# Performance work log

Measured on AMD Instinct MI355X. Metric: run time of the kernel, lower is better.

The kernel has to match this reference:

```python
import jax, jax.numpy as jnp
import numpy as np

B, WS, DIM, HEADS, AGENT, PS = 128, 14, 256, 8, 49, 7
N = WS * WS


def conv(x, w, b, pad, groups=1):
    y = jax.lax.conv_general_dilated(x, w, (1, 1), [(pad, pad), (pad, pad)],
                                     dimension_numbers=('NCHW', 'OIHW', 'NCHW'),
                                     feature_group_count=groups)
    return y + b[None, :, None, None]


def bilinear_resize(x, oh, ow):
    # F.interpolate(mode='bilinear', align_corners=False) on last two dims
    ih, iw = x.shape[-2], x.shape[-1]
    def grid(ni, no):
        pos = np.maximum((np.arange(no) + 0.5) * (ni / no) - 0.5, 0.0)
        i0 = np.minimum(np.floor(pos).astype(np.int32), ni - 1)
        i1 = np.minimum(i0 + 1, ni - 1)
        return i0, i1, (pos - i0).astype(np.float32)
    i0h, i1h, lh = grid(ih, oh)
    i0w, i1w, lw = grid(iw, ow)
    xh = x[..., i0h, :] * (1.0 - lh)[:, None] + x[..., i1h, :] * lh[:, None]
    return xh[..., i0w] * (1.0 - lw) + xh[..., i1w] * lw


def rel_pos_index(h, w):
    coords = np.stack(np.meshgrid(np.arange(h), np.arange(w), indexing='ij')).reshape(2, -1)
    rel = (coords[:, :, None] - coords[:, None, :]).transpose(1, 2, 0).copy()
    rel[..., 0] += h - 1
    rel[..., 1] += w - 1
    rel[..., 0] *= 2 * w - 1
    return rel.sum(-1)  # (h*w, h*w)


def cbam(x, caa1_w, caa1_b, caa2_w, caa2_b, cam1_w, cam1_b, cam2_w, cam2_b, sa_w, sa_b):
    # ChannelAttention: both conv stacks act on 1x1 pooled maps -> only kernel centers matter
    avgp = x.mean((2, 3))
    t1 = jax.nn.relu(jnp.einsum('oi,bi->bo', caa1_w[:, :, 1, 1], avgp) + caa1_b)
    y1 = jax.nn.sigmoid(jnp.einsum('oi,bi->bo', caa2_w[:, :, 1, 1], t1) + caa2_b)
    mxp = x.max((2, 3))
    t2 = jax.nn.relu(jnp.einsum('oi,bi->bo', cam1_w[:, :, 0, 0], mxp) + cam1_b)
    y2 = jax.nn.sigmoid(jnp.einsum('oi,bi->bo', cam2_w[:, :, 0, 0], t2) + cam2_b)
    x = jax.nn.sigmoid(y1 + y2)[:, :, None, None] * x
    # Spatial attention
    mask = jnp.concatenate([x.mean(1, keepdims=True), x.max(1, keepdims=True)], axis=1)
    mask = jax.nn.sigmoid(conv(mask, sa_w, sa_b, 4))
    return x * mask


def chan_inter(x, ci1_w, ci1_b, bn_g, bn_b, ci2_w, ci2_b):
    # AdaptiveAvgPool2d(1) then 5x5 convs on 1x1 maps -> kernel-center matmuls; BN in eval mode
    p = x.mean((2, 3))
    t = jnp.einsum('oi,bi->bo', ci1_w[:, :, 2, 2], p) + ci1_b
    t = jax.nn.relu(bn_g * t * (1.0 / np.sqrt(1.0 + 1e-5)) + bn_b)
    return jnp.einsum('oi,bi->bo', ci2_w[:, :, 2, 2], t) + ci2_b


def setup_inputs() -> dict:
    key = jax.random.key(0)
    ks = jax.random.split(key, 40)
    d, r = DIM, DIM // 16
    p = lambda i, shape, s=0.02: jax.random.normal(ks[i], shape, jnp.float32) * s
    return {
        'x': jax.random.normal(ks[0], (B, N, d), jnp.float32),
        'h': WS,
        'w': WS,
        'lka_w': p(1, (3 * d, 1, 5, 5)), 'lka_b': p(2, (3 * d,)),
        'conv5_w': p(3, (d, d, 5, 5)), 'conv5_b': p(4, (d,)),
        'caa1_w': p(5, (r, d, 3, 3)), 'caa1_b': p(6, (r,)),
        'caa2_w': p(7, (d, r, 3, 3)), 'caa2_b': p(8, (d,)),
        'cam1_w': p(9, (r, d, 1, 1)), 'cam1_b': p(10, (r,)),
        'cam2_w': p(11, (d, r, 1, 1)), 'cam2_b': p(12, (d,)),
        'sa_w': p(13, (1, 2, 9, 9)), 'sa_b': p(14, (1,)),
        'ci1_w': p(15, (r, d, 5, 5)), 'ci1_b': p(16, (r,)),
        'bn_g': jnp.ones((r,), jnp.float32), 'bn_b': jnp.zeros((r,), jnp.float32),
        'ci2_w': p(17, (d, r, 5, 5)), 'ci2_b': p(18, (d,)),
        'rpb_table': p(19, ((2 * WS - 1) * (2 * WS - 1), HEADS)),
        'an_bias': p(20, (HEADS, AGENT, 7, 7)), 'na_bias': p(21, (HEADS, AGENT, 7, 7)),
        'ah_bias': p(22, (1, HEADS, AGENT, WS, 1)), 'aw_bias': p(23, (1, HEADS, AGENT, 1, WS)),
        'ha_bias': p(24, (1, HEADS, WS, 1, AGENT)), 'wa_bias': p(25, (1, HEADS, 1, WS, AGENT)),
        'dwc_w': p(26, (d, 1, 5, 5)), 'dwc_b': p(27, (d,)),
        'proj_w': p(28, (d, d)), 'proj_b': p(29, (d,)),
    }


def reference(x, h, w, lka_w, lka_b, conv5_w, conv5_b, caa1_w, caa1_b, caa2_w, caa2_b,
              cam1_w, cam1_b, cam2_w, cam2_b, sa_w, sa_b, ci1_w, ci1_b, bn_g, bn_b,
              ci2_w, ci2_b, rpb_table, an_bias, na_bias, ah_bias, aw_bias, ha_bias,
              wa_bias, dwc_w, dwc_b, proj_w, proj_b):
    b, n, c = x.shape
    heads, agent, ps = HEADS, AGENT, PS
    hd = c // heads
    scale = hd ** (-0.5)

    xc = jnp.transpose(x.reshape(b, h, w, c), (0, 3, 1, 2))  # (b,c,h,w)
    y = conv(xc, lka_w, lka_b, 2, groups=c)                   # depthwise, 3 outputs/group
    k_raw, v_raw, q_raw = y[:, :c], y[:, c:2 * c], y[:, 2 * c:]

    # v branch: conv5 then raw reshape-scramble (faithful to torch .reshape of NCHW), then CBAM
    v5 = jnp.transpose(conv(v_raw, conv5_w, conv5_b, 2).reshape(b, h, w, c), (0, 3, 1, 2))
    vc = cbam(v5, caa1_w, caa1_b, caa2_w, caa2_b, cam1_w, cam1_b, cam2_w, cam2_b, sa_w, sa_b)
    v_feat = jnp.transpose(vc.reshape(b, c, n), (0, 2, 1))    # (b,n,c)

    # adaptive avg/max pool 14->7 == exact 2x2 pooling
    at = q_raw.reshape(b, c, ps, h // ps, ps, w // ps).mean((3, 5)).reshape(b, c, agent).transpose(0, 2, 1)
    atk = k_raw.reshape(b, c, ps, h // ps, ps, w // ps).max((3, 5)).reshape(b, c, agent).transpose(0, 2, 1)

    # raw row-major reshapes of (b,c,h,w) into (b,n,heads,hd): faithful to torch
    q = q_raw.reshape(b, n, heads, hd).transpose(0, 2, 1, 3) * scale
    k = k_raw.reshape(b, n, heads, hd).transpose(0, 2, 1, 3)
    v = v_raw.reshape(b, n, heads, hd).transpose(0, 2, 1, 3)
    v1 = v_feat.reshape(b, n, heads, hd).transpose(0, 2, 1, 3)

    # full window attention with relative position bias
    idx = rel_pos_index(h, w)
    rpb = rpb_table[idx.reshape(-1)].reshape(n, n, heads).transpose(2, 0, 1)
    attn = jax.nn.softmax(jnp.einsum('bhid,bhjd->bhij', q, k) + rpb[None])
    x1 = jnp.einsum('bhij,bhjd->bhid', attn, v).transpose(0, 2, 1, 3).reshape(b, n, c)

    ar = x1.transpose(0, 2, 1).reshape(b, c, h, w)
    cmap = chan_inter(ar, ci1_w, ci1_b, bn_g, bn_b, ci2_w, ci2_b)  # (b,c)
    conv_x2 = jax.nn.sigmoid(cmap)[:, :, None, None] * jnp.transpose(q.reshape(b, h, w, c), (0, 3, 1, 2))

    # agent attention
    at_h = at.reshape(b, agent, heads, hd).transpose(0, 2, 1, 3)
    atk_h = atk.reshape(b, agent, heads, hd).transpose(0, 2, 1, 3)
    pb = bilinear_resize(an_bias, h, w).reshape(1, heads, agent, n) \
         + (ah_bias + aw_bias).reshape(1, heads, agent, n)
    agent_attn = jax.nn.softmax(jnp.einsum('bhad,bhnd->bhan', at_h * scale, k) + pb)
    agent_attn1 = jax.nn.softmax(jnp.einsum('bhad,bhnd->bhan', atk_h * scale, q) + pb)
    agent_v = jnp.einsum('bhan,bhnd->bhad', agent_attn, v1) + jnp.einsum('bhan,bhnd->bhad', agent_attn1, v)

    ab = bilinear_resize(na_bias, h, w).reshape(1, heads, agent, n).transpose(0, 1, 3, 2) \
         + (ha_bias + wa_bias).reshape(1, heads, n, agent)
    q_attn = jax.nn.softmax(jnp.einsum('bhnd,bhad->bhna', q * scale, at_h) + ab)
    k_attn = jax.nn.softmax(jnp.einsum('bhnd,bhad->bhna', k * scale, atk_h) + ab)
    xo = jnp.einsum('bhna,bhad->bhnd', q_attn + k_attn, agent_v).transpose(0, 2, 1, 3).reshape(b, n, c)

    xo = xo + jnp.transpose(conv(conv_x2, dwc_w, dwc_b, 2, groups=c), (0, 2, 3, 1)).reshape(b, n, c)
    qc = jnp.transpose(q.transpose(0, 2, 1, 3).reshape(b, h, w, c), (0, 3, 1, 2))
    xo = xo + jnp.transpose(conv(qc, dwc_w, dwc_b, 2, groups=c), (0, 2, 3, 1)).reshape(b, n, c)

    return xo @ proj_w.T + proj_b
```

## Files before the change

kernel.cpp:

```cpp
#include <hip/hip_runtime.h>

#define NB    128
#define NC    256
#define NPOS  196
#define NHEAD 8
#define NAG   49
#define YSTR  150528
#define VOFF  50176
#define QOFF  100352
#define SCL   0.17677669529663687f

#define WS_Y    0u
#define WS_V5   19267584u
#define WS_AT   25690112u
#define WS_ATK  27295744u
#define WS_CHG  28901376u
#define WS_CMAP 28934144u
#define WS_PBT  28966912u
#define WS_AB   29043744u
#define WS_X1S  29120576u
#define WS_AGV  29153344u
#define WS_XO   30758976u
#define WS_WT   37181504u
#define WS_CWT  37247040u

typedef __attribute__((ext_vector_type(8))) _Float16 half8;
typedef __attribute__((ext_vector_type(8))) short short8;
typedef __attribute__((ext_vector_type(4))) short short4v;
typedef __attribute__((ext_vector_type(4))) float f32x4;
typedef unsigned short ushort_t;
typedef unsigned int uint_t;

__device__ __forceinline__ float sigmoidf_(float x){ return 1.0f/(1.0f+__expf(-x)); }

__device__ __forceinline__ ushort_t f2h(float x){
  _Float16 h = (_Float16)x; return __builtin_bit_cast(ushort_t, h);
}
__device__ __forceinline__ float h2f(ushort_t u){
  return (float)__builtin_bit_cast(_Float16, u);
}

__device__ __forceinline__ float bilin7(const float* __restrict__ src, int i, int j){
  float pi = fmaxf(0.5f*(float)i - 0.25f, 0.f);
  int i0 = (int)pi; if (i0 > 6) i0 = 6;
  int i1 = i0 + 1;  if (i1 > 6) i1 = 6;
  float li = pi - (float)i0;
  float pj = fmaxf(0.5f*(float)j - 0.25f, 0.f);
  int j0 = (int)pj; if (j0 > 6) j0 = 6;
  int j1 = j0 + 1;  if (j1 > 6) j1 = 6;
  float lj = pj - (float)j0;
  float v00 = src[i0*7+j0], v01 = src[i0*7+j1];
  float v10 = src[i1*7+j0], v11 = src[i1*7+j1];
  float t0 = v00*(1.f-lj) + v01*lj;
  float t1 = v10*(1.f-lj) + v11*lj;
  return t0*(1.f-li) + t1*li;
}

__device__ __forceinline__ void conv5x5_row(const float* __restrict__ plane, int r,
                                            const float* __restrict__ w25, float* acc14){
  #pragma unroll
  for (int di = 0; di < 5; ++di){
    const float4* pr = (const float4*)(plane + (r+di)*20);
    float4 p0 = pr[0], p1 = pr[1], p2 = pr[2], p3 = pr[3], p4 = pr[4];
    float row[20] = {p0.x,p0.y,p0.z,p0.w, p1.x,p1.y,p1.z,p1.w, p2.x,p2.y,p2.z,p2.w,
                     p3.x,p3.y,p3.z,p3.w, p4.x,p4.y,p4.z,p4.w};
    #pragma unroll
    for (int dj = 0; dj < 5; ++dj){
      float w = w25[di*5+dj];
      #pragma unroll
      for (int j = 0; j < 14; ++j) acc14[j] = fmaf(row[j+dj], w, acc14[j]);
    }
  }
}

__global__ void k_pb(const float* __restrict__ an, const float* __restrict__ ah,
                     const float* __restrict__ aw, float* __restrict__ PBT){
  int t = blockIdx.x*256 + threadIdx.x;
  if (t >= NHEAD*NPOS*NAG) return;
  int a = t % NAG;
  int r = t / NAG;
  int n = r % NPOS;
  int h = r / NPOS;
  int i = n/14, j = n - (n/14)*14;
  float v = bilin7(an + ((size_t)h*NAG + a)*49, i, j);
  v += ah[((size_t)h*NAG + a)*14 + i] + aw[((size_t)h*NAG + a)*14 + j];
  PBT[t] = v;
}

__global__ void k_ab(const float* __restrict__ na, const float* __restrict__ ha,
                     const float* __restrict__ wa, float* __restrict__ AB){
  int t = blockIdx.x*256 + threadIdx.x;
  if (t >= NHEAD*NPOS*NAG) return;
  int a = t % NAG;
  int r = t / NAG;
  int n = r % NPOS;
  int h = r / NPOS;
  int i = n/14, j = n - (n/14)*14;
  float v = bilin7(na + ((size_t)h*NAG + a)*49, i, j);
  v += ha[((size_t)h*14 + i)*NAG + a] + wa[((size_t)h*14 + j)*NAG + a];
  AB[t] = v;
}

__global__ void k_wt(const float* __restrict__ pw, float* __restrict__ WT){
  int t = blockIdx.x*256 + threadIdx.x;
  if (t >= 65536) return;
  int k = t >> 8, c = t & 255;
  WT[t] = pw[c*256 + k];
}

__global__ void k_cw2(const float* __restrict__ cw, ushort_t* __restrict__ Wh){
  int t = blockIdx.x*256 + threadIdx.x;
  if (t >= 1638400) return;
  int ci = t & 255;
  int r  = t >> 8;
  int co = r & 255;
  int tap = r >> 8;
  Wh[t] = f2h(cw[((size_t)co*256 + ci)*25 + tap]);
}

__global__ __launch_bounds__(256) void k_lka(const float* __restrict__ x, const float* __restrict__ lw,
                                             const float* __restrict__ lb, float* __restrict__ Y){
  int b = blockIdx.x >> 3, gb = blockIdx.x & 7;
  int g0 = gb*32;
  __shared__ __align__(16) float pl[32*360];
  int tid = threadIdx.x;
  for (int t = tid; t < 32*360; t += 256) pl[t] = 0.f;
  __syncthreads();
  for (int t = tid; t < 32*196; t += 256){
    int gl = t & 31, s = t >> 5;
    int i = s/14, j = s - i*14;
    pl[gl*360 + (i+2)*20 + j + 2] = x[((size_t)b*196 + s)*256 + g0 + gl];
  }
  __syncthreads();
  for (int t = tid; t < 96*14; t += 256){
    int ocl = t/14, r = t - ocl*14;
    int o  = g0*3 + ocl;
    int gl = ocl/3;
    float w25[25];
    #pragma unroll
    for (int u = 0; u < 25; ++u) w25[u] = lw[o*25 + u];
    float acc[14];
    float bv = lb[o];
    #pragma unroll
    for (int j = 0; j < 14; ++j) acc[j] = bv;
    conv5x5_row(&pl[gl*360], r, w25, acc);
    float* dst = Y + ((size_t)b*768 + o)*196 + r*14;
    #pragma unroll
    for (int j = 0; j < 14; ++j) dst[j] = acc[j];
  }
}

__global__ __launch_bounds__(256, 2) void k_conv5(const float* __restrict__ Y,
    const ushort_t* __restrict__ Wh, const float* __restrict__ cb, float* __restrict__ V5){
  int b = blockIdx.x >> 2, cog = blockIdx.x & 3;
  int co0 = cog*64;
  __shared__ __align__(16) ushort_t Pt[360*40];
  __shared__ __align__(16) ushort_t Wsm[5*64*40];
  __shared__ float T[32*200];
  int tid  = threadIdx.x;
  int lane = tid & 63, wv = tid >> 6;
  int mrow = lane & 15, quad = lane >> 4;

  for (int t = tid; t < 7200; t += 256) ((uint_t*)Pt)[t] = 0;

  int prow[4];
  #pragma unroll
  for (int mt = 0; mt < 4; ++mt){
    int s = wv*64 + mt*16 + mrow;
    int p0 = 0;
    if (s < 196){ int i = s/14, j = s - i*14; p0 = i*20 + j; }
    prow[mt] = p0;
  }

  f32x4 acc[4][4];
  #pragma unroll
  for (int mt = 0; mt < 4; ++mt)
    #pragma unroll
    for (int nt = 0; nt < 4; ++nt) acc[mt][nt] = (f32x4){0.f,0.f,0.f,0.f};

  const float* src = Y + (size_t)b*YSTR + VOFF;
  int wco = tid >> 2, wpart = tid & 3;

  #pragma unroll 1
  for (int cc = 0; cc < 8; ++cc){
    __syncthreads();
    for (int t = tid; t < 3136; t += 256){
      int cp = t / 196, s = t - cp*196;
      int i = s/14, j = s - i*14;
      const float* s0 = src + (size_t)(cc*32 + 2*cp)*196 + s;
      float v0 = s0[0];
      float v1 = s0[196];
      ((uint_t*)Pt)[((i+2)*20 + j + 2)*20 + cp] =
          (uint_t)f2h(v0) | ((uint_t)f2h(v1) << 16);
    }
    #pragma unroll 1
    for (int di = 0; di < 5; ++di){
      __syncthreads();
      #pragma unroll
      for (int tp = 0; tp < 5; ++tp){
        int tap = di*5 + tp;
        const short8 g = *(const short8*)(Wh + ((size_t)tap*256 + co0 + wco)*256 + cc*32 + wpart*8);
        *(short8*)&Wsm[(tp*64 + wco)*40 + wpart*8] = g;
      }
      __syncthreads();
      #pragma unroll
      for (int dj = 0; dj < 5; ++dj){
        half8 a[4], bb[4];
        #pragma unroll
        for (int nt = 0; nt < 4; ++nt){
          int co = nt*16 + mrow;
          bb[nt] = *(const half8*)&Wsm[(dj*64 + co)*40 + quad*8];
        }
        #pragma unroll
        for (int mt = 0; mt < 4; ++mt){
          int p = prow[mt] + di*20 + dj;
          a[mt] = *(const half8*)&Pt[p*40 + quad*8];
        }
        #pragma unroll
        for (int mt = 0; mt < 4; ++mt)
          #pragma unroll
          for (int nt = 0; nt < 4; ++nt)
            acc[mt][nt] = __builtin_amdgcn_mfma_f32_16x16x32_f16(a[mt], bb[nt], acc[mt][nt], 0, 0, 0);
      }
    }
  }

  #pragma unroll
  for (int hf = 0; hf < 2; ++hf){
    __syncthreads();
    #pragma unroll
    for (int ntl = 0; ntl < 2; ++ntl){
      int nt = hf*2 + ntl;
      int col = ntl*16 + mrow;
      #pragma unroll
      for (int mt = 0; mt < 4; ++mt){
        int sbase = wv*64 + mt*16 + quad*4;
        #pragma unroll
        for (int r = 0; r < 4; ++r){
          int s = sbase + r;
          if (s < 196) T[col*200 + s] = acc[mt][nt][r];
        }
      }
    }
    __syncthreads();
    for (int t = tid; t < 6272; t += 256){
      int cl = t / 196;
      int f = (co0 + hf*32)*196 + t;
      float val = T[t + cl*4] + cb[co0 + hf*32 + cl];
      V5[(size_t)b*50176 + (size_t)(f & 255)*196 + (f >> 8)] = val;
    }
  }
}

__global__ __launch_bounds__(256) void k_pool(const float* __restrict__ Y, float* __restrict__ AT, float* __restrict__ ATK){
  int b = blockIdx.x; int c = threadIdx.x;
  const float* qp = Y + ((size_t)b*768 + 512 + c)*196;
  const float* kp = Y + ((size_t)b*768 + c)*196;
  for (int a = 0; a < 49; ++a){
    int p1 = a/7, p2 = a - p1*7;
    int s = p1*28 + p2*2;
    float q0 = qp[s], q1 = qp[s+1], q2 = qp[s+14], q3 = qp[s+15];
    AT[((size_t)b*49 + a)*256 + c] = 0.25f*(q0+q1+q2+q3);
    float k0 = kp[s], k1 = kp[s+1], k2 = kp[s+14], k3 = kp[s+15];
    ATK[((size_t)b*49 + a)*256 + c] = fmaxf(fmaxf(k0,k1), fmaxf(k2,k3));
  }
}

__global__ __launch_bounds__(256) void k_cbam_a(const float* __restrict__ V5,
    const float* __restrict__ caa1w, const float* __restrict__ caa1b,
    const float* __restrict__ caa2w, const float* __restrict__ caa2b,
    const float* __restrict__ cam1w, const float* __restrict__ cam1b,
    const float* __restrict__ cam2w, const float* __restrict__ cam2b,
    float* __restrict__ CHG){
  int b = blockIdx.x, c = threadIdx.x;
  __shared__ float avg[256], mx[256], t1[16], t2[16];
  const float* pp = V5 + ((size_t)b*256 + c)*196;
  float s = 0.f, m = -1e30f;
  for (int i = 0; i < 196; ++i){ float v = pp[i]; s += v; m = fmaxf(m, v); }
  avg[c] = s * (1.0f/196.0f); mx[c] = m;
  __syncthreads();
  if (c < 16){
    float a1 = caa1b[c], a2 = cam1b[c];
    #pragma unroll 4
    for (int k = 0; k < 256; ++k){
      a1 = fmaf(caa1w[(c*256 + k)*9 + 4], avg[k], a1);
      a2 = fmaf(cam1w[c*256 + k], mx[k], a2);
    }
    t1[c] = fmaxf(a1, 0.f);
    t2[c] = fmaxf(a2, 0.f);
  }
  __syncthreads();
  float y1 = caa2b[c], y2 = cam2b[c];
  #pragma unroll
  for (int k = 0; k < 16; ++k){
    y1 = fmaf(caa2w[(c*16 + k)*9 + 4], t1[k], y1);
    y2 = fmaf(cam2w[c*16 + k], t2[k], y2);
  }
  CHG[b*256 + c] = sigmoidf_(sigmoidf_(y1) + sigmoidf_(y2));
}

__global__ __launch_bounds__(256) void k_cbam_b(float* __restrict__ V5, const float* __restrict__ CHG,
    const float* __restrict__ saw, const float* __restrict__ sab){
  int b = blockIdx.x; int tid = threadIdx.x;
  __shared__ float chg[256];
  __shared__ float mp[22*22], xp[22*22];
  __shared__ float mk[196];
  chg[tid] = CHG[b*256 + tid];
  for (int t = tid; t < 484; t += 256){ mp[t] = 0.f; xp[t] = 0.f; }
  __syncthreads();
  if (tid < 196){
    int i = tid/14, j = tid - i*14;
    float s = 0.f, m = -1e30f;
    const float* vb = V5 + (size_t)b*256*196 + tid;
    for (int c = 0; c < 256; ++c){
      float v = chg[c] * vb[c*196];
      s += v; m = fmaxf(m, v);
    }
    mp[(i+4)*22 + j+4] = s*(1.f/256.f);
    xp[(i+4)*22 + j+4] = m;
  }
  __syncthreads();
  if (tid < 196){
    int i = tid/14, j = tid - i*14;
    float acc = sab[0];
    for (int di = 0; di < 9; ++di){
      #pragma unroll
      for (int dj = 0; dj < 9; ++dj){
        acc = fmaf(mp[(i+di)*22 + j+dj], saw[di*9+dj], acc);
        acc = fmaf(xp[(i+di)*22 + j+dj], saw[81 + di*9+dj], acc);
      }
    }
    mk[tid] = sigmoidf_(acc);
  }
  __syncthreads();
  if (tid < 196){
    float m = mk[tid];
    float* vb = V5 + (size_t)b*256*196 + tid;
    for (int c = 0; c < 256; ++c) vb[c*196] = chg[c]*vb[c*196]*m;
  }
}

__global__ __launch_bounds__(256) void k_attn(const float* __restrict__ Y, const float* __restrict__ rpbt,
                                              float* __restrict__ X1S){
  int b = blockIdx.x >> 3, h = blockIdx.x & 7;
  __shared__ float rp[729];
  __shared__ float xs[196*33];
  int tid = threadIdx.x;
  for (int t = tid; t < 729; t += 256) rp[t] = rpbt[t*8 + h];
  __syncthreads();
  const float* yb = Y + (size_t)b*YSTR;
  if (tid < 196){
    int n = tid;
    float q[32];
    {
      const float4* q4 = (const float4*)(yb + QOFF + (size_t)n*256 + h*32);
      #pragma unroll
      for (int u = 0; u < 8; ++u){
        float4 v = q4[u];
        q[4*u] = v.x*SCL; q[4*u+1] = v.y*SCL; q[4*u+2] = v.z*SCL; q[4*u+3] = v.w*SCL;
      }
    }
    int ri = n/14, ci = n - ri*14;
    int bidx = (ri + 13)*27 + (ci + 13);
    float acc[32];
    #pragma unroll
    for (int d = 0; d < 32; ++d) acc[d] = 0.f;
    float l = 0.f;
    int rj = 0, cj = 0;
    for (int j = 0; j < 196; ++j){
      const float4* k4 = (const float4*)(yb + (size_t)j*256 + h*32);
      float s0 = 0.f, s1 = 0.f;
      #pragma unroll
      for (int u = 0; u < 8; u += 2){
        float4 a = k4[u], bb = k4[u+1];
        s0 = fmaf(q[4*u+0],a.x, fmaf(q[4*u+1],a.y, fmaf(q[4*u+2],a.z, fmaf(q[4*u+3],a.w, s0))));
        s1 = fmaf(q[4*u+4],bb.x, fmaf(q[4*u+5],bb.y, fmaf(q[4*u+6],bb.z, fmaf(q[4*u+7],bb.w, s1))));
      }
      float s = s0 + s1 + rp[bidx - rj*27 - cj];
      float p = __expf(s);
      l += p;
      const float4* v4 = (const float4*)(yb + VOFF + (size_t)j*256 + h*32);
      #pragma unroll
      for (int u = 0; u < 8; ++u){
        float4 vv = v4[u];
        acc[4*u]   = fmaf(p, vv.x, acc[4*u]);
        acc[4*u+1] = fmaf(p, vv.y, acc[4*u+1]);
        acc[4*u+2] = fmaf(p, vv.z, acc[4*u+2]);
        acc[4*u+3] = fmaf(p, vv.w, acc[4*u+3]);
      }
      if (++cj == 14){ cj = 0; ++rj; }
    }
    float inv = 1.f/l;
    #pragma unroll
    for (int d = 0; d < 32; ++d) xs[n*33 + d] = acc[d]*inv;
  }
  __syncthreads();
  if (tid < 32){
    float s = 0.f;
    for (int n = 0; n < 196; ++n) s += xs[n*33 + tid];
    X1S[(size_t)b*256 + h*32 + tid] = s*(1.f/196.f);
  }
}

__global__ __launch_bounds__(256) void k_cinter(const float* __restrict__ X1S,
    const float* __restrict__ ci1w, const float* __restrict__ ci1b,
    const float* __restrict__ bng, const float* __restrict__ bnb,
    const float* __restrict__ ci2w, const float* __restrict__ ci2b, float* __restrict__ CMAP){
  int b = blockIdx.x, c = threadIdx.x;
  __shared__ float p[256], tt[16];
  p[c] = X1S[b*256 + c];
  __syncthreads();
  if (c < 16){
    float a = ci1b[c];
    #pragma unroll 4
    for (int k = 0; k < 256; ++k) a = fmaf(ci1w[(c*256+k)*25 + 12], p[k], a);
    const float invs = 0.9999950000375f;
    tt[c] = fmaxf(fmaf(bng[c]*invs, a, bnb[c]), 0.f);
  }
  __syncthreads();
  float a = ci2b[c];
  #pragma unroll
  for (int k = 0; k < 16; ++k) a = fmaf(ci2w[(c*16+k)*25 + 12], tt[k], a);
  CMAP[b*256 + c] = sigmoidf_(a);
}

__global__ __launch_bounds__(256) void k_agentv(const float* __restrict__ Y, const float* __restrict__ V5,
    const float* __restrict__ AT, const float* __restrict__ ATK,
    const float* __restrict__ PBT, float* __restrict__ AGV){
  int b = blockIdx.x >> 3, h = blockIdx.x & 7;
  __shared__ __align__(16) ushort_t ST[64*232];
  __shared__ __align__(16) ushort_t R[8704];
  __shared__ float psum[4*64];
  __shared__ float inv0s[64], inv1s[64];
  int tid = threadIdx.x, wv = tid >> 6, lane = tid & 63;
  int mrow = lane & 15, quad = lane >> 4;
  int sw8 = ((quad ^ ((mrow >> 1) & 3)) << 3);
  const float* yb = Y + (size_t)b*YSTR;
  ushort_t* Kh = R;
  ushort_t* Ah = R + 6656;
  ushort_t* Vt = R;
  f32x4 out0[2], out1[2];

  for (int t = tid; t < 512; t += 256){
    int a = t >> 3, c2 = 208 + ((t & 7) << 1);
    *(uint_t*)&ST[a*232 + c2] = 0;
  }

  #pragma unroll 1
  for (int pass = 0; pass < 2; ++pass){
    for (int t = tid; t < 192; t += 256) ((uint_t*)Kh)[3136 + t] = 0;
    for (int t = tid; t < 240; t += 256) ((uint_t*)Ah)[784 + t] = 0;
    {
      const float* rsrc = yb + (pass ? QOFF : 0) + h*32;
      for (int t = tid; t < 3136; t += 256){
        int n = t >> 4, w = t & 15;
        const float2 v = *(const float2*)(rsrc + (size_t)n*256 + (w << 1));
        int ws = (((w >> 2) ^ ((n >> 1) & 3)) << 2) | (w & 3);
        ((uint_t*)Kh)[n*16 + ws] = (uint_t)f2h(v.x) | ((uint_t)f2h(v.y) << 16);
      }
      const float* asrc = (pass ? ATK : AT) + (size_t)b*49*256 + h*32;
      for (int t = tid; t < 784; t += 256){
        int a = t >> 4, w = t & 15;
        const float2 v = *(const float2*)(asrc + (size_t)a*256 + (w << 1));
        int ws = (((w >> 2) ^ ((a >> 1) & 3)) << 2) | (w & 3);
        ((uint_t*)Ah)[a*16 + ws] = (uint_t)f2h(v.x) | ((uint_t)f2h(v.y) << 16);
      }
    }
    __syncthreads();
    {
      float lscl = pass ? 0.03125f : SCL;
      int ag = wv*16 + mrow;
      half8 bfr = *(const half8*)&Ah[ag*32 + sw8];
      #pragma unroll 1
      for (int mt = 0; mt < 13; ++mt){
        half8 afr = *(const half8*)&Kh[(mt*16 + mrow)*32 + sw8];
        f32x4 c = (f32x4){0.f,0.f,0.f,0.f};
        c = __builtin_amdgcn_mfma_f32_16x16x32_f16(afr, bfr, c, 0, 0, 0);
        int n0 = mt*16 + quad*4;
        short4v pk;
        #pragma unroll
        for (int r = 0; r < 4; ++r){
          int n = n0 + r;
          float pb = PBT[((size_t)h*196 + n)*49 + ag];
          float e = (n < 196) ? __expf(fmaf(c[r], lscl, pb)) : 0.f;
          pk[r] = (short)f2h(e);
        }
        *(short4v*)&ST[ag*232 + n0] = pk;
      }
    }
    __syncthreads();
    {
      int a = tid >> 2, q = tid & 3;
      float s = 0.f;
      #pragma unroll
      for (int u = 0; u < 7; ++u){
        short8 v8 = *(const short8*)&ST[a*232 + q*56 + u*8];
        #pragma unroll
        for (int e = 0; e < 8; ++e) s += h2f((ushort_t)v8[e]);
      }
      psum[q*64 + a] = s;
    }
    if (pass == 0){
      const float* vsrc = V5 + (size_t)b*50176 + h*32*196;
      for (int t = tid; t < 3136; t += 256){
        int d = t / 98, np = t - (t/98)*98;
        const float2 v = *(const float2*)(vsrc + (size_t)d*196 + 2*np);
        *(uint_t*)&Vt[d*232 + 2*np] = (uint_t)f2h(v.x) | ((uint_t)f2h(v.y) << 16);
      }
    } else {
      const float* vsrc = yb + VOFF + h*32;
      for (int t = tid; t < 3136; t += 256){
        int d = t / 98, np = t - (t/98)*98;
        float v0 = vsrc[(size_t)(2*np)*256 + d];
        float v1 = vsrc[(size_t)(2*np+1)*256 + d];
        *(uint_t*)&Vt[d*232 + 2*np] = (uint_t)f2h(v0) | ((uint_t)f2h(v1) << 16);
      }
    }
    for (int t = tid; t < 448; t += 256){
      int d = t / 14, c2 = 196 + 2*(t - (t/14)*14);
      *(uint_t*)&Vt[d*232 + c2] = 0;
    }
    __syncthreads();
    {
      f32x4* outp = pass ? out1 : out0;
      #pragma unroll
      for (int nt = 0; nt < 2; ++nt){
        f32x4 c = (f32x4){0.f,0.f,0.f,0.f};
        #pragma unroll
        for (int ks = 0; ks < 7; ++ks){
          half8 afr = *(const half8*)&ST[(wv*16 + mrow)*232 + ks*32 + quad*8];
          half8 bfr = *(const half8*)&Vt[(nt*16 + mrow)*232 + ks*32 + quad*8];
          c = __builtin_amdgcn_mfma_f32_16x16x32_f16(afr, bfr, c, 0, 0, 0);
        }
        outp[nt] = c;
      }
      if (tid < 64){
        float s = psum[tid] + psum[64+tid] + psum[128+tid] + psum[192+tid];
        float* invp = pass ? inv1s : inv0s;
        invp[tid] = 1.f / s;
      }
    }
    __syncthreads();
  }
  #pragma unroll
  for (int nt = 0; nt < 2; ++nt){
    int d = nt*16 + mrow;
    #pragma unroll
    for (int r = 0; r < 4; ++r){
      int a = wv*16 + quad*4 + r;
      if (a < 49)
        AGV[(((size_t)(b*8 + h)*49) + a)*32 + d] = out0[nt][r]*inv0s[a] + out1[nt][r]*inv1s[a];
    }
  }
}

__global__ __launch_bounds__(256) void k_xo1(const float* __restrict__ Y,
    const float* __restrict__ AT, const float* __restrict__ ATK,
    const float* __restrict__ AB, const float* __restrict__ AGV, float* __restrict__ XO){
  int b = blockIdx.x >> 3, h = blockIdx.x & 7;
  __shared__ __align__(16) ushort_t ST[208*72];
  __shared__ __align__(16) ushort_t Kh[208*32];
  __shared__ __align__(16) ushort_t Ah[64*32];
  __shared__ __align__(16) ushort_t AGVt[32*64];
  __shared__ float invs[208];
  int tid = threadIdx.x, wv = tid >> 6, lane = tid & 63;
  int mrow = lane & 15, quad = lane >> 4;
  int sw8 = ((quad ^ ((mrow >> 1) & 3)) << 3);
  const float* yb = Y + (size_t)b*YSTR;
  f32x4 acc[4][2];
  #pragma unroll
  for (int i = 0; i < 4; ++i){
    acc[i][0] = (f32x4){0.f,0.f,0.f,0.f};
    acc[i][1] = (f32x4){0.f,0.f,0.f,0.f};
  }

  for (int t = tid; t < 1664; t += 256){
    int rw = t >> 3, c2 = 48 + ((t & 7) << 1);
    *(uint_t*)&ST[rw*72 + c2] = 0;
  }
  {
    const float* agvb = AGV + (size_t)(b*8 + h)*49*32;
    for (int t = tid; t < 2048; t += 256){
      int d = t >> 6, a = t & 63;
      int as = ((((a >> 3) ^ (d & 7)) & 7) << 3) | (a & 7);
      AGVt[d*64 + as] = (a < 49) ? f2h(agvb[a*32 + d]) : (ushort_t)0;
    }
  }

  #pragma unroll 1
  for (int pass = 0; pass < 2; ++pass){
    {
      const float* rsrc = yb + (pass ? 0 : QOFF) + h*32;
      for (int t = tid; t < 3136; t += 256){
        int n = t >> 4, w = t & 15;
        const float2 v = *(const float2*)(rsrc + (size_t)n*256 + (w << 1));
        int ws = (((w >> 2) ^ ((n >> 1) & 3)) << 2) | (w & 3);
        ((uint_t*)Kh)[n*16 + ws] = (uint_t)f2h(v.x) | ((uint_t)f2h(v.y) << 16);
      }
      const float* asrc = (pass ? ATK : AT) + (size_t)b*49*256 + h*32;
      for (int t = tid; t < 784; t += 256){
        int a = t >> 4, w = t & 15;
        const float2 v = *(const float2*)(asrc + (size_t)a*256 + (w << 1));
        int ws = (((w >> 2) ^ ((a >> 1) & 3)) << 2) | (w & 3);
        ((uint_t*)Ah)[a*16 + ws] = (uint_t)f2h(v.x) | ((uint_t)f2h(v.y) << 16);
      }
    }
    __syncthreads();
    {
      float lscl = pass ? SCL : 0.03125f;
      int ag = wv*16 + mrow;
      half8 bfr = *(const half8*)&Ah[ag*32 + sw8];
      #pragma unroll 1
      for (int mt = 0; mt < 13; ++mt){
        half8 afr = *(const half8*)&Kh[(mt*16 + mrow)*32 + sw8];
        f32x4 c = (f32x4){0.f,0.f,0.f,0.f};
        c = __builtin_amdgcn_mfma_f32_16x16x32_f16(afr, bfr, c, 0, 0, 0);
        #pragma unroll
        for (int r = 0; r < 4; ++r){
          int n = mt*16 + quad*4 + r;
          if (n < 196 && ag < 49){
            float e = __expf(fmaf(c[r], lscl, AB[((size_t)h*196 + n)*49 + ag]));
            ST[n*72 + ag] = f2h(e);
          }
        }
      }
    }
    __syncthreads();
    if (tid < 196){
      float s = 0.f;
      #pragma unroll
      for (int u = 0; u < 7; ++u){
        short8 v8 = *(const short8*)&ST[tid*72 + u*8];
        #pragma unroll
        for (int e = 0; e < 8; ++e) s += h2f((ushort_t)v8[e]);
      }
      invs[tid] = 1.f / s;
    }
    __syncthreads();
    {
      int i = 0;
      #pragma unroll 1
      for (int mt = wv; mt < 13; mt += 4, ++i){
        #pragma unroll
        for (int nt = 0; nt < 2; ++nt){
          f32x4 c = (f32x4){0.f,0.f,0.f,0.f};
          #pragma unroll
          for (int ks = 0; ks < 2; ++ks){
            half8 afr = *(const half8*)&ST[(mt*16 + mrow)*72 + ks*32 + quad*8];
            half8 bfr = *(const half8*)&AGVt[(nt*16 + mrow)*64 + ((((ks*4 + quad) ^ (mrow & 7)) & 7) << 3)];
            c = __builtin_amdgcn_mfma_f32_16x16x32_f16(afr, bfr, c, 0, 0, 0);
          }
          #pragma unroll
          for (int r = 0; r < 4; ++r){
            int n = mt*16 + quad*4 + r;
            if (n < 196) acc[i][nt][r] = fmaf(c[r], invs[n], acc[i][nt][r]);
          }
        }
      }
    }
    __syncthreads();
  }
  {
    int i = 0;
    #pragma unroll 1
    for (int mt = wv; mt < 13; mt += 4, ++i){
      #pragma unroll
      for (int nt = 0; nt < 2; ++nt){
        #pragma unroll
        for (int r = 0; r < 4; ++r){
          int n = mt*16 + quad*4 + r;
          if (n < 196)
            XO[((size_t)b*196 + n)*256 + h*32 + nt*16 + mrow] = acc[i][nt][r];
        }
      }
    }
  }
}

__global__ __launch_bounds__(256) void k_dwc(const float* __restrict__ Y, const float* __restrict__ CMAP,
    const float* __restrict__ dw, const float* __restrict__ db, float* __restrict__ XO){
  int b = blockIdx.x >> 3, cg = blockIdx.x & 7;
  int c0 = cg*32;
  __shared__ __align__(16) float pl[32*360];
  int tid = threadIdx.x;
  for (int t = tid; t < 32*360; t += 256) pl[t] = 0.f;
  __syncthreads();
  const float* yq = Y + (size_t)b*YSTR + QOFF;
  for (int t = tid; t < 32*196; t += 256){
    int cl = t & 31, s = t >> 5;
    int c = c0 + cl;
    int G = s*256 + c;
    int hh = G / 6272;
    int rem = G - hh*6272;
    int n = rem >> 5, d = rem & 31;
    float cx2 = CMAP[b*256 + c] * yq[n*256 + hh*32 + d];
    float qc  = yq[G];
    float v = SCL*(cx2 + qc);
    int i = s/14, j = s - i*14;
    pl[cl*360 + (i+2)*20 + j + 2] = v;
  }
  __syncthreads();
  for (int t = tid; t < 32*14; t += 256){
    int cl = t/14, r = t - cl*14;
    int c = c0 + cl;
    float w25[25];
    #pragma unroll
    for (int u = 0; u < 25; ++u) w25[u] = dw[c*25 + u];
    float acc[14];
    float b2 = 2.f*db[c];
    #pragma unroll
    for (int j = 0; j < 14; ++j) acc[j] = b2;
    conv5x5_row(&pl[cl*360], r, w25, acc);
    float* dst = XO + ((size_t)b*196 + r*14)*256 + c;
    #pragma unroll
    for (int j = 0; j < 14; ++j) dst[j*256] += acc[j];
  }
}

__global__ __launch_bounds__(256) void k_proj(const float* __restrict__ XO, const float* __restrict__ WT,
    const float* __restrict__ pbias, float* __restrict__ OUT){
  int bb = blockIdx.x / 7, nt = blockIdx.x % 7;
  int n0 = nt*28;
  int c = threadIdx.x;
  const float* xb = XO + ((size_t)bb*196 + n0)*256;
  float acc[28];
  #pragma unroll
  for (int r = 0; r < 28; ++r) acc[r] = 0.f;
  for (int k = 0; k < 256; k += 4){
    float w0 = WT[(k+0)*256 + c];
    float w1 = WT[(k+1)*256 + c];
    float w2 = WT[(k+2)*256 + c];
    float w3 = WT[(k+3)*256 + c];
    #pragma unroll
    for (int r = 0; r < 28; ++r){
      float4 xv = *(const float4*)(xb + r*256 + k);
      acc[r] = fmaf(xv.x, w0, fmaf(xv.y, w1, fmaf(xv.z, w2, fmaf(xv.w, w3, acc[r]))));
    }
  }
  float bv = pbias[c];
  float* dst = OUT + ((size_t)bb*196 + n0)*256 + c;
  #pragma unroll
  for (int r = 0; r < 28; ++r) dst[r*256] = acc[r] + bv;
}

extern "C" void kernel_launch(void* const* d_in, const int* in_sizes, int n_in,
                              void* d_out, int out_size, void* d_ws, size_t ws_size,
                              hipStream_t stream){
  (void)in_sizes; (void)n_in; (void)out_size; (void)ws_size;
  const float* x       = (const float*)d_in[0];
  const float* lka_w   = (const float*)d_in[3];
  const float* lka_b   = (const float*)d_in[4];
  const float* conv5_w = (const float*)d_in[5];
  const float* conv5_b = (const float*)d_in[6];
  const float* caa1_w  = (const float*)d_in[7];
  const float* caa1_b  = (const float*)d_in[8];
  const float* caa2_w  = (const float*)d_in[9];
  const float* caa2_b  = (const float*)d_in[10];
  const float* cam1_w  = (const float*)d_in[11];
  const float* cam1_b  = (const float*)d_in[12];
  const float* cam2_w  = (const float*)d_in[13];
  const float* cam2_b  = (const float*)d_in[14];
  const float* sa_w    = (const float*)d_in[15];
  const float* sa_b    = (const float*)d_in[16];
  const float* ci1_w   = (const float*)d_in[17];
  const float* ci1_b   = (const float*)d_in[18];
  const float* bn_g    = (const float*)d_in[19];
  const float* bn_b    = (const float*)d_in[20];
  const float* ci2_w   = (const float*)d_in[21];
  const float* ci2_b   = (const float*)d_in[22];
  const float* rpbt    = (const float*)d_in[23];
  const float* an_bias = (const float*)d_in[24];
  const float* na_bias = (const float*)d_in[25];
  const float* ah_bias = (const float*)d_in[26];
  const float* aw_bias = (const float*)d_in[27];
  const float* ha_bias = (const float*)d_in[28];
  const float* wa_bias = (const float*)d_in[29];
  const float* dwc_w   = (const float*)d_in[30];
  const float* dwc_b   = (const float*)d_in[31];
  const float* proj_w  = (const float*)d_in[32];
  const float* proj_b  = (const float*)d_in[33];
  float* out = (float*)d_out;
  float* ws = (float*)d_ws;

  float* Y    = ws + WS_Y;
  float* V5   = ws + WS_V5;
  float* AT   = ws + WS_AT;
  float* ATK  = ws + WS_ATK;
  float* CHG  = ws + WS_CHG;
  float* CMAP = ws + WS_CMAP;
  float* PBT  = ws + WS_PBT;
  float* AB   = ws + WS_AB;
  float* X1S  = ws + WS_X1S;
  float* AGV  = ws + WS_AGV;
  float* XO   = ws + WS_XO;
  float* WT   = ws + WS_WT;
  ushort_t* Wh = (ushort_t*)(ws + WS_CWT);

  k_pb   <<<301, 256, 0, stream>>>(an_bias, ah_bias, aw_bias, PBT);
  k_ab   <<<301, 256, 0, stream>>>(na_bias, ha_bias, wa_bias, AB);
  k_wt   <<<256, 256, 0, stream>>>(proj_w, WT);
  k_cw2  <<<6400, 256, 0, stream>>>(conv5_w, Wh);
  k_lka  <<<1024, 256, 0, stream>>>(x, lka_w, lka_b, Y);
  k_conv5<<<512, 256, 0, stream>>>(Y, Wh, conv5_b, V5);
  k_pool <<<128, 256, 0, stream>>>(Y, AT, ATK);
  k_cbam_a<<<128, 256, 0, stream>>>(V5, caa1_w, caa1_b, caa2_w, caa2_b,
                                    cam1_w, cam1_b, cam2_w, cam2_b, CHG);
  k_cbam_b<<<128, 256, 0, stream>>>(V5, CHG, sa_w, sa_b);
  k_attn <<<1024, 256, 0, stream>>>(Y, rpbt, X1S);
  k_cinter<<<128, 256, 0, stream>>>(X1S, ci1_w, ci1_b, bn_g, bn_b, ci2_w, ci2_b, CMAP);
  k_agentv<<<1024, 256, 0, stream>>>(Y, V5, AT, ATK, PBT, AGV);
  k_xo1  <<<1024, 256, 0, stream>>>(Y, AT, ATK, AB, AGV, XO);
  k_dwc  <<<1024, 256, 0, stream>>>(Y, CMAP, dwc_w, dwc_b, XO);
  k_proj <<<896, 256, 0, stream>>>(XO, WT, proj_b, out);
}
```

Baseline: 895.4 us.

## Rewrite window attention with MFMA scores and mean-pooled reassociation; swizzle conv5 LDS

The window attention kernel now computes QK^T scores with fp16 MFMA, stores unnormalised exponentials in LDS, and uses the fact that only the mean over queries is needed. It sums the normalised attention weights per key first, then does a single weighted sum over V, which replaces the per-query PV accumulation. The conv5 kernel gets XOR-swizzled LDS layouts for the patch and weight tiles to avoid bank conflicts, a packed per-position staging loop, and skips the MFMAs for the padded rows in the last wave. This trades fp32 precision for fp16 in the scores and uses much more shared memory per block.

After: 870.0 us. -2.8%, faster.

```diff
diff --git a/kernel.cpp b/kernel.cpp
--- a/kernel.cpp
+++ b/kernel.cpp
@@ -160,6 +160,7 @@
   int tid  = threadIdx.x;
   int lane = tid & 63, wv = tid >> 6;
   int mrow = lane & 15, quad = lane >> 4;
+  int mtN  = (wv < 3) ? 4 : 1;
 
   for (int t = tid; t < 7200; t += 256) ((uint_t*)Pt)[t] = 0;
 
@@ -184,14 +185,18 @@
   #pragma unroll 1
   for (int cc = 0; cc < 8; ++cc){
     __syncthreads();
-    for (int t = tid; t < 3136; t += 256){
-      int cp = t / 196, s = t - cp*196;
-      int i = s/14, j = s - i*14;
-      const float* s0 = src + (size_t)(cc*32 + 2*cp)*196 + s;
-      float v0 = s0[0];
-      float v1 = s0[196];
-      ((uint_t*)Pt)[((i+2)*20 + j + 2)*20 + cp] =
-          (uint_t)f2h(v0) | ((uint_t)f2h(v1) << 16);
+    if (tid < 196){
+      int s = tid; int i = s/14, j = s - i*14;
+      int p = (i+2)*20 + (j+2);
+      const float* s0 = src + (cc*32)*196 + s;
+      #pragma unroll
+      for (int cp = 0; cp < 16; ++cp){
+        float v0 = s0[(2*cp)*196];
+        float v1 = s0[(2*cp+1)*196];
+        uint_t pk = (uint_t)f2h(v0) | ((uint_t)f2h(v1) << 16);
+        int q = cp >> 2;
+        *(uint_t*)&Pt[p*40 + (((q ^ p) & 3) << 3) + ((2*cp) & 7)] = pk;
+      }
     }
     #pragma unroll 1
     for (int di = 0; di < 5; ++di){
@@ -200,7 +205,7 @@
       for (int tp = 0; tp < 5; ++tp){
         int tap = di*5 + tp;
         const short8 g = *(const short8*)(Wh + ((size_t)tap*256 + co0 + wco)*256 + cc*32 + wpart*8);
-        *(short8*)&Wsm[(tp*64 + wco)*40 + wpart*8] = g;
+        *(short8*)&Wsm[(tp*64 + wco)*40 + (((wpart ^ wco) & 3) << 3)] = g;
       }
       __syncthreads();
       #pragma unroll
@@ -209,18 +214,23 @@
         #pragma unroll
         for (int nt = 0; nt < 4; ++nt){
           int co = nt*16 + mrow;
-          bb[nt] = *(const half8*)&Wsm[(dj*64 + co)*40 + quad*8];
+          bb[nt] = *(const half8*)&Wsm[(dj*64 + co)*40 + (((quad ^ co) & 3) << 3)];
         }
         #pragma unroll
         for (int mt = 0; mt < 4; ++mt){
-          int p = prow[mt] + di*20 + dj;
-          a[mt] = *(const half8*)&Pt[p*40 + quad*8];
+          if (mt < mtN){
+            int p = prow[mt] + di*20 + dj;
+            a[mt] = *(const half8*)&Pt[p*40 + (((quad ^ p) & 3) << 3)];
+          }
         }
         #pragma unroll
-        for (int mt = 0; mt < 4; ++mt)
-          #pragma unroll
-          for (int nt = 0; nt < 4; ++nt)
-            acc[mt][nt] = __builtin_amdgcn_mfma_f32_16x16x32_f16(a[mt], bb[nt], acc[mt][nt], 0, 0, 0);
+        for (int mt = 0; mt < 4; ++mt){
+          if (mt < mtN){
+            #pragma unroll
+            for (int nt = 0; nt < 4; ++nt)
+              acc[mt][nt] = __builtin_amdgcn_mfma_f32_16x16x32_f16(a[mt], bb[nt], acc[mt][nt], 0, 0, 0);
+          }
+        }
       }
     }
   }
@@ -340,64 +350,125 @@
   }
 }
 
-__global__ __launch_bounds__(256) void k_attn(const float* __restrict__ Y, const float* __restrict__ rpbt,
-                                              float* __restrict__ X1S){
+__global__ __launch_bounds__(512, 1) void k_attn2(const float* __restrict__ Y,
+    const float* __restrict__ rpbt, float* __restrict__ X1S){
   int b = blockIdx.x >> 3, h = blockIdx.x & 7;
-  __shared__ float rp[729];
-  __shared__ float xs[196*33];
-  int tid = threadIdx.x;
-  for (int t = tid; t < 729; t += 256) rp[t] = rpbt[t*8 + h];
-  __syncthreads();
+  __shared__ __align__(16) ushort_t Qh[208*32];
+  __shared__ __align__(16) ushort_t Kh[208*32];
+  __shared__ __align__(16) ushort_t E[196*208];
+  __shared__ float rp[736];
+  __shared__ int   rpo[208];
+  __shared__ float lnn[208];
+  __shared__ float invl[196];
+  __shared__ float wj[208];
+  __shared__ float wpart[14][208];
+  __shared__ float xpart[16][32];
+  int tid = threadIdx.x, wv = tid >> 6, lane = tid & 63;
+  int mrow = lane & 15, quad = lane >> 4;
+  int sw8 = ((quad ^ ((mrow >> 1) & 3)) << 3);
   const float* yb = Y + (size_t)b*YSTR;
-  if (tid < 196){
-    int n = tid;
-    float q[32];
-    {
-      const float4* q4 = (const float4*)(yb + QOFF + (size_t)n*256 + h*32);
-      #pragma unroll
-      for (int u = 0; u < 8; ++u){
-        float4 v = q4[u];
-        q[4*u] = v.x*SCL; q[4*u+1] = v.y*SCL; q[4*u+2] = v.z*SCL; q[4*u+3] = v.w*SCL;
-      }
-    }
-    int ri = n/14, ci = n - ri*14;
-    int bidx = (ri + 13)*27 + (ci + 13);
-    float acc[32];
-    #pragma unroll
-    for (int d = 0; d < 32; ++d) acc[d] = 0.f;
-    float l = 0.f;
-    int rj = 0, cj = 0;
-    for (int j = 0; j < 196; ++j){
-      const float4* k4 = (const float4*)(yb + (size_t)j*256 + h*32);
-      float s0 = 0.f, s1 = 0.f;
-      #pragma unroll
-      for (int u = 0; u < 8; u += 2){
-        float4 a = k4[u], bb = k4[u+1];
-        s0 = fmaf(q[4*u+0],a.x, fmaf(q[4*u+1],a.y, fmaf(q[4*u+2],a.z, fmaf(q[4*u+3],a.w, s0))));
-        s1 = fmaf(q[4*u+4],bb.x, fmaf(q[4*u+5],bb.y, fmaf(q[4*u+6],bb.z, fmaf(q[4*u+7],bb.w, s1))));
-      }
-      float s = s0 + s1 + rp[bidx - rj*27 - cj];
-      float p = __expf(s);
-      l += p;
-      const float4* v4 = (const float4*)(yb + VOFF + (size_t)j*256 + h*32);
-      #pragma unroll
-      for (int u = 0; u < 8; ++u){
-        float4 vv = v4[u];
-        acc[4*u]   = fmaf(p, vv.x, acc[4*u]);
-        acc[4*u+1] = fmaf(p, vv.y, acc[4*u+1]);
-        acc[4*u+2] = fmaf(p, vv.z, acc[4*u+2]);
-        acc[4*u+3] = fmaf(p, vv.w, acc[4*u+3]);
-      }
-      if (++cj == 14){ cj = 0; ++rj; }
-    }
-    float inv = 1.f/l;
-    #pragma unroll
-    for (int d = 0; d < 32; ++d) xs[n*33 + d] = acc[d]*inv;
+
+  for (int t = tid; t < 736; t += 512) rp[t] = (t < 729) ? rpbt[t*8 + h] : 0.f;
+  for (int j = tid; j < 208; j += 512){
+    int jc = (j < 196) ? j : 195;
+    int rj = jc/14;
+    rpo[j] = rj*27 + (jc - rj*14);
+  }
+  for (int t = tid; t < 384; t += 512){
+    int arr = t >= 192; int u = t - arr*192;
+    ((uint_t*)(arr ? Kh : Qh))[3136 + u] = 0;
+  }
+  for (int t = tid; t < 3136; t += 512){
+    int n = t >> 4, w = t & 15;
+    int ws = (((w >> 2) ^ ((n >> 1) & 3)) << 2) | (w & 3);
+    const float2 qv = *(const float2*)(yb + QOFF + (size_t)n*256 + h*32 + (w << 1));
+    ((uint_t*)Qh)[n*16 + ws] = (uint_t)f2h(qv.x*SCL) | ((uint_t)f2h(qv.y*SCL) << 16);
+    const float2 kv = *(const float2*)(yb + (size_t)n*256 + h*32 + (w << 1));
+    ((uint_t*)Kh)[n*16 + ws] = (uint_t)f2h(kv.x) | ((uint_t)f2h(kv.y) << 16);
+  }
+  __syncthreads();
+
+  #pragma unroll 1
+  for (int nc = wv; nc < 13; nc += 8){
+    int n = nc*16 + mrow;
+    half8 bfr = *(const half8*)&Qh[n*32 + sw8];
+    int nclamp = (n < 196) ? n : 195;
+    int rin = nclamp/14, cin = nclamp - rin*14;
+    int bidxn = (rin + 13)*27 + (cin + 13);
+    float lsum = 0.f;
+    #pragma unroll 1
+    for (int mt = 0; mt < 13; ++mt){
+      half8 afr = *(const half8*)&Kh[(mt*16 + mrow)*32 + sw8];
+      f32x4 c = (f32x4){0.f,0.f,0.f,0.f};
+      c = __builtin_amdgcn_mfma_f32_16x16x32_f16(afr, bfr, c, 0, 0, 0);
+      int j0 = mt*16 + quad*4;
+      int4 ro = *(const int4*)&rpo[j0];
+      short4v pk;
+      #pragma unroll
+      for (int r = 0; r < 4; ++r){
+        int j = j0 + r;
+        int roff = (r == 0) ? ro.x : (r == 1) ? ro.y : (r == 2) ? ro.z : ro.w;
+        float e = (j < 196) ? __expf(c[r] + rp[bidxn - roff]) : 0.f;
+        lsum += e;
+        pk[r] = (short)f2h(e);
+      }
+      if (n < 196) *(short4v*)&E[n*208 + j0] = pk;
+    }
+    lsum += __shfl_xor(lsum, 16);
+    lsum += __shfl_xor(lsum, 32);
+    if (quad == 0) lnn[n] = lsum;
+  }
+  __syncthreads();
+  for (int n = tid; n < 196; n += 512) invl[n] = 1.f/lnn[n];
+  __syncthreads();
+
+  {
+    int g = tid >> 5, lj = tid & 31;
+    int j0 = lj*8;
+    if (g < 14 && j0 < 208){
+      float a0=0.f,a1=0.f,a2=0.f,a3=0.f,a4=0.f,a5=0.f,a6=0.f,a7=0.f;
+      #pragma unroll 1
+      for (int u = 0; u < 14; ++u){
+        int n = g*14 + u;
+        float iv = invl[n];
+        short8 ev = *(const short8*)&E[n*208 + j0];
+        a0 = fmaf(h2f((ushort_t)ev[0]), iv, a0);
+        a1 = fmaf(h2f((ushort_t)ev[1]), iv, a1);
+        a2 = fmaf(h2f((ushort_t)ev[2]), iv, a2);
+        a3 = fmaf(h2f((ushort_t)ev[3]), iv, a3);
+        a4 = fmaf(h2f((ushort_t)ev[4]), iv, a4);
+        a5 = fmaf(h2f((ushort_t)ev[5]), iv, a5);
+        a6 = fmaf(h2f((ushort_t)ev[6]), iv, a6);
+        a7 = fmaf(h2f((ushort_t)ev[7]), iv, a7);
+      }
+      *(f32x4*)&wpart[g][j0]   = (f32x4){a0,a1,a2,a3};
+      *(f32x4*)&wpart[g][j0+4] = (f32x4){a4,a5,a6,a7};
+    }
+  }
+  __syncthreads();
+  for (int j = tid; j < 208; j += 512){
+    float s = 0.f;
+    #pragma unroll
+    for (int g2 = 0; g2 < 14; ++g2) s += wpart[g2][j];
+    wj[j] = (j < 196) ? s : 0.f;
+  }
+  __syncthreads();
+
+  {
+    int d = tid & 31, g = tid >> 5;
+    float s = 0.f;
+    #pragma unroll 1
+    for (int u = 0; u < 13; ++u){
+      int j = g*13 + u;
+      s = fmaf(wj[j], yb[VOFF + (size_t)j*256 + h*32 + d], s);
+    }
+    xpart[g][d] = s;
   }
   __syncthreads();
   if (tid < 32){
     float s = 0.f;
-    for (int n = 0; n < 196; ++n) s += xs[n*33 + tid];
+    #pragma unroll
+    for (int g2 = 0; g2 < 16; ++g2) s += xpart[g2][tid];
     X1S[(size_t)b*256 + h*32 + tid] = s*(1.f/196.f);
   }
 }
@@ -806,7 +877,7 @@
   k_cbam_a<<<128, 256, 0, stream>>>(V5, caa1_w, caa1_b, caa2_w, caa2_b,
                                     cam1_w, cam1_b, cam2_w, cam2_b, CHG);
   k_cbam_b<<<128, 256, 0, stream>>>(V5, CHG, sa_w, sa_b);
-  k_attn <<<1024, 256, 0, stream>>>(Y, rpbt, X1S);
+  k_attn2<<<1024, 512, 0, stream>>>(Y, rpbt, X1S);
   k_cinter<<<128, 256, 0, stream>>>(X1S, ci1_w, ci1_b, bn_g, bn_b, ci2_w, ci2_b, CMAP);
   k_agentv<<<1024, 256, 0, stream>>>(Y, V5, AT, ATK, PBT, AGV);
   k_xo1  <<<1024, 256, 0, stream>>>(Y, AT, ATK, AB, AGV, XO);
```
